# Kernel tuning notes

Measured on AMD Instinct MI355X. Metric: run time of the kernel, lower is better.

The kernel has to match this reference:

```python
import jax, jax.numpy as jnp
import numpy as np

B, L, ENC, D, H, HD, MLP, R = 4, 512, 512, 1024, 16, 64, 4096, 32
NUM_BUCKETS, MAX_DISTANCE = 32, 128
EPS = 1e-6
NEG = -1e10


def rmsnorm(x, scale):
    var = jnp.mean(jnp.square(x), axis=-1, keepdims=True)
    return x * jax.lax.rsqrt(var + EPS) * scale


def rel_pos_bias(table, qlen, klen):
    # T5 causal (bidirectional=False) relative position bucketing.
    ctx = jnp.arange(qlen)[:, None]
    mem = jnp.arange(klen)[None, :]
    rp = mem - ctx                      # [q, k]
    n = -jnp.minimum(rp, 0)             # distance into the past
    max_exact = NUM_BUCKETS // 2
    is_small = n < max_exact
    large = max_exact + (
        jnp.log(jnp.maximum(n, 1).astype(jnp.float32) / max_exact)
        / np.log(MAX_DISTANCE / max_exact) * (NUM_BUCKETS - max_exact)
    ).astype(jnp.int32)
    large = jnp.minimum(large, NUM_BUCKETS - 1)
    bucket = jnp.where(is_small, n, large)
    return table[bucket].transpose(2, 0, 1)[None]  # [1, h, q, k]


def lora_dense(x, W, a, b):
    # x:[B,L,d]  W:[d,e]  a:[B,d,r]  b:[B,r,e]  -> xW + (xa)b per example
    out = jnp.einsum('bld,de->ble', x, W)
    low = jnp.einsum('bld,bdr->blr', x, a)
    return out + jnp.einsum('blr,bre->ble', low, b)


def attention(xq, xkv, Wq, Wk, Wv, Wo, qa, qb, ka, kb, va, vb, oa, ob, bias):
    b, ql, _ = xq.shape
    kl = xkv.shape[1]
    q = lora_dense(xq, Wq, qa, qb).reshape(b, ql, H, HD) * (1.0 / np.sqrt(HD))
    k = lora_dense(xkv, Wk, ka, kb).reshape(b, kl, H, HD)
    v = lora_dense(xkv, Wv, va, vb).reshape(b, kl, H, HD)
    scores = jnp.einsum('bqhd,bkhd->bhqk', q, k)
    if bias is not None:
        scores = scores + bias
    probs = jax.nn.softmax(scores, axis=-1)
    ctx = jnp.einsum('bhqk,bkhd->bqhd', probs, v).reshape(b, ql, H * HD)
    return lora_dense(ctx, Wo, oa, ob)


def setup_inputs() -> dict:
    key = jax.random.key(0)
    ks = jax.random.split(key, 32)
    s = 0.02
    inp = {
        'inputs':  jax.random.normal(ks[0], (B, L, D), jnp.float32),
        'encoded': jax.random.normal(ks[1], (B, ENC, D), jnp.float32),
        'lora_qa': jax.random.normal(ks[2], (B, 2, D, R), jnp.float32) * s,
        'lora_qb': jax.random.normal(ks[3], (B, 2, R, D), jnp.float32) * s,
        'lora_ka': jax.random.normal(ks[4], (B, 2, D, R), jnp.float32) * s,
        'lora_kb': jax.random.normal(ks[5], (B, 2, R, D), jnp.float32) * s,
        'lora_va': jax.random.normal(ks[6], (B, 2, D, R), jnp.float32) * s,
        'lora_vb': jax.random.normal(ks[7], (B, 2, R, D), jnp.float32) * s,
        'lora_oa': jax.random.normal(ks[8], (B, 2, D, R), jnp.float32) * s,
        'lora_ob': jax.random.normal(ks[9], (B, 2, R, D), jnp.float32) * s,
        'rel_table': jax.random.normal(ks[10], (NUM_BUCKETS, H), jnp.float32) * s,
        'ln1': jnp.ones((D,), jnp.float32),
        'ln2': jnp.ones((D,), jnp.float32),
        'ln3': jnp.ones((D,), jnp.float32),
        'sWq': jax.random.normal(ks[11], (D, H * HD), jnp.float32) * s,
        'sWk': jax.random.normal(ks[12], (D, H * HD), jnp.float32) * s,
        'sWv': jax.random.normal(ks[13], (D, H * HD), jnp.float32) * s,
        'sWo': jax.random.normal(ks[14], (H * HD, D), jnp.float32) * s,
        'cWq': jax.random.normal(ks[15], (D, H * HD), jnp.float32) * s,
        'cWk': jax.random.normal(ks[16], (D, H * HD), jnp.float32) * s,
        'cWv': jax.random.normal(ks[17], (D, H * HD), jnp.float32) * s,
        'cWo': jax.random.normal(ks[18], (H * HD, D), jnp.float32) * s,
        'wi0': jax.random.normal(ks[19], (D, MLP), jnp.float32) * s,
        'wi1': jax.random.normal(ks[20], (D, MLP), jnp.float32) * s,
        'wo_mlp': jax.random.normal(ks[21], (MLP, D), jnp.float32) * s,
    }
    return inp


def reference(inputs, encoded, lora_qa, lora_qb, lora_ka, lora_kb, lora_va, lora_vb,
              lora_oa, lora_ob, rel_table, ln1, ln2, ln3,
              sWq, sWk, sWv, sWo, cWq, cWk, cWv, cWo, wi0, wi1, wo_mlp):
    l = inputs.shape[1]
    causal = jnp.tril(jnp.ones((l, l), dtype=bool))
    dec_bias = rel_pos_bias(rel_table, l, l) + jnp.where(causal, 0.0, NEG)[None, None]

    # --- self-attention block ---
    x = rmsnorm(inputs, ln1)
    x = attention(x, x, sWq, sWk, sWv, sWo,
                  lora_qa[:, 0], lora_qb[:, 0], lora_ka[:, 0], lora_kb[:, 0],
                  lora_va[:, 0], lora_vb[:, 0], lora_oa[:, 0], lora_ob[:, 0],
                  dec_bias)
    x = x + inputs

    # --- cross-attention block ---
    y = rmsnorm(x, ln2)
    y = attention(y, encoded, cWq, cWk, cWv, cWo,
                  lora_qa[:, 1], lora_qb[:, 1], lora_ka[:, 1], lora_kb[:, 1],
                  lora_va[:, 1], lora_vb[:, 1], lora_oa[:, 1], lora_ob[:, 1],
                  None)
    y = y + x

    # --- gated-gelu MLP block (T5 v1.1 style) ---
    lz = rmsnorm(y, ln3)
    h = jax.nn.gelu(lz @ wi0, approximate=False) * (lz @ wi1)
    z = h @ wo_mlp + y
    return z
```

## Files before the change

### kernel.cpp

```cpp
#include <hip/hip_runtime.h>
#include <math.h>


#define DEV __device__ __forceinline__

typedef __bf16 bf16x8 __attribute__((ext_vector_type(8)));
typedef float floatx4 __attribute__((ext_vector_type(4)));

typedef __attribute__((address_space(1))) void* gas_ptr;
typedef __attribute__((address_space(3))) void* las_ptr;

DEV unsigned short f2bf(float f) {
  union { float f; unsigned int u; } v; v.f = f;
  unsigned int r = v.u + 0x7fffu + ((v.u >> 16) & 1u);
  return (unsigned short)(r >> 16);
}
DEV float bf2f(unsigned short u) {
  union { unsigned int u; float f; } v; v.u = ((unsigned int)u) << 16;
  return v.f;
}

#define GLOAD_LDS16(g, l) __builtin_amdgcn_global_load_lds((gas_ptr)(g), (las_ptr)(l), 16, 0, 0)

template<int NW>
DEV void stage_tile_sw(const char* gbase, char* lds, int nrows, int ldbytes, int wave, int lane) {
  int nchunks = nrows >> 3;
  int colb = (((lane & 7) ^ ((lane >> 3) & 7)) << 4);
  for (int c = wave; c < nchunks; c += NW) {
    int row = (c << 3) + (lane >> 3);
    GLOAD_LDS16(gbase + (size_t)row * ldbytes + colb, lds + (c << 10));
  }
}

template<int NW>
DEV void stage_tile256_sw(const char* gbase, char* lds, int nrows, int ldbytes, int wave, int lane) {
  int nchunks = nrows >> 2;
  for (int c = wave; c < nchunks; c += NW) {
    int row = (c << 2) + (lane >> 4);
    int key = row & 7;
    int colb = ((lane & 15) ^ key) << 4;
    GLOAD_LDS16(gbase + (size_t)row * ldbytes + colb, lds + (c << 10));
  }
}

template<int WM, int WN>
DEV void gemm_core(const unsigned short* A, const unsigned short* Bt, float* C,
                   int K, int lda, int ldb, int ldc, int m0, int n0,
                   char* ldsA, char* ldsB) {
  constexpr int NW = WM * WN;
  const int tid  = threadIdx.x;
  const int lane = tid & 63;
  const int wave = tid >> 6;
  const int wm   = wave % WM;
  const int wn   = wave / WM;
  const int quad = lane >> 4;
  const int l15  = lane & 15;
  const int key  = l15 & 7;

  floatx4 acc[4][4];
#pragma unroll
  for (int i = 0; i < 4; ++i)
#pragma unroll
    for (int j = 0; j < 4; ++j) acc[i][j] = (floatx4){0.f, 0.f, 0.f, 0.f};

  const char* gA = (const char*)(A + (size_t)m0 * lda);
  const char* gB = (const char*)(Bt + (size_t)n0 * ldb);

  for (int k0 = 0; k0 < K; k0 += 64) {
    stage_tile_sw<NW>(gA + (size_t)k0 * 2, ldsA, WM * 64, lda * 2, wave, lane);
    stage_tile_sw<NW>(gB + (size_t)k0 * 2, ldsB, WN * 64, ldb * 2, wave, lane);
    __syncthreads();
#pragma unroll
    for (int kk = 0; kk < 64; kk += 32) {
      bf16x8 af[4], bv[4];
      int off = (((kk >> 3) + quad) ^ key) << 4;
      const char* baseA = ldsA + (size_t)(wm * 64 + l15) * 128 + off;
      const char* baseB = ldsB + (size_t)(wn * 64 + l15) * 128 + off;
#pragma unroll
      for (int mi = 0; mi < 4; ++mi) af[mi] = *(const bf16x8*)(baseA + mi * 2048);
#pragma unroll
      for (int ni = 0; ni < 4; ++ni) bv[ni] = *(const bf16x8*)(baseB + ni * 2048);
#pragma unroll
      for (int mi = 0; mi < 4; ++mi)
#pragma unroll
        for (int ni = 0; ni < 4; ++ni)
          acc[mi][ni] = __builtin_amdgcn_mfma_f32_16x16x32_bf16(af[mi], bv[ni], acc[mi][ni], 0, 0, 0);
    }
    __syncthreads();
  }

#pragma unroll
  for (int mi = 0; mi < 4; ++mi) {
#pragma unroll
    for (int r = 0; r < 4; ++r) {
      int row = m0 + wm * 64 + mi * 16 + quad * 4 + r;
#pragma unroll
// ... 51 lines not shown
      stage_tile_sw<4>((const char*)sl.A0 + (size_t)m0 * 2048 + it * 128, ldsA, 128, 2048, wave, lane);
      stage_tile_sw<4>((const char*)sl.B0 + (size_t)n0 * 2048 + it * 128, ldsB, 128, 2048, wave, lane);
    } else {
      int eb = (it - 16) * 128;
      stage_tile_sw<4>((const char*)sl.Aext + (size_t)m0 * 256 + eb, ldsA, 128, 256, wave, lane);
      stage_tile_sw<4>((const char*)(sl.Bext + (size_t)b * sl.bextb) + (size_t)n0 * 256 + eb,
                       ldsB, 128, 256, wave, lane);
    }
    __syncthreads();
#pragma unroll
    for (int kk = 0; kk < 64; kk += 32) {
      bf16x8 af[4], bv[4];
      int off = (((kk >> 3) + quad) ^ key) << 4;
      const char* baseA = ldsA + (size_t)(wm * 64 + l15) * 128 + off;
      const char* baseB = ldsB + (size_t)(wn * 64 + l15) * 128 + off;
#pragma unroll
      for (int mi = 0; mi < 4; ++mi) af[mi] = *(const bf16x8*)(baseA + mi * 2048);
#pragma unroll
      for (int ni = 0; ni < 4; ++ni) bv[ni] = *(const bf16x8*)(baseB + ni * 2048);
#pragma unroll
      for (int mi = 0; mi < 4; ++mi)
#pragma unroll
        for (int ni = 0; ni < 4; ++ni)
          acc[mi][ni] = __builtin_amdgcn_mfma_f32_16x16x32_bf16(af[mi], bv[ni], acc[mi][ni], 0, 0, 0);
    }
    __syncthreads();
  }

#pragma unroll
  for (int mi = 0; mi < 4; ++mi) {
#pragma unroll
    for (int r = 0; r < 4; ++r) {
      int row = m0 + wm * 64 + mi * 16 + quad * 4 + r;
#pragma unroll
      for (int ni = 0; ni < 4; ++ni) {
        int col = n0 + wn * 64 + ni * 16 + l15;
        sl.C[(size_t)row * sl.ldc + col] = acc[mi][ni][r];
      }
    }
  }
}

struct QKVSlice {
  const unsigned short* A0;
  const unsigned short* Aext;
  const unsigned short* B0;
  const unsigned short* Bext;
  unsigned short* sec0;
  unsigned short* sec1;
  unsigned short* sec2;
  size_t bextb;
  int vsec, nxa;
};
struct QKV2 { QKVSlice s[2]; };

__global__ __launch_bounds__(256) void k_gemmqkv(QKV2 g) {
  __shared__ char lds[34816];
  char* ldsA = lds;
  char* ldsB = lds + 16384;
  QKVSlice sl = g.s[blockIdx.z];
  if ((int)blockIdx.x >= sl.nxa) return;
  const int m0 = blockIdx.y * 128, n0 = blockIdx.x * 128;
  const int b = m0 >> 9;
  const int tid = threadIdx.x, lane = tid & 63, wave = tid >> 6;
  const int wm = wave & 1, wn = wave >> 1;
  const int quad = lane >> 4, l15 = lane & 15;
  const int key = l15 & 7;

  floatx4 acc[4][4];
#pragma unroll
  for (int i = 0; i < 4; ++i)
#pragma unroll
    for (int j = 0; j < 4; ++j) acc[i][j] = (floatx4){0.f, 0.f, 0.f, 0.f};

  for (int it = 0; it < 18; ++it) {
    if (it < 16) {
      stage_tile_sw<4>((const char*)sl.A0 + (size_t)m0 * 2048 + it * 128, ldsA, 128, 2048, wave, lane);
      stage_tile_sw<4>((const char*)sl.B0 + (size_t)n0 * 2048 + it * 128, ldsB, 128, 2048, wave, lane);
    } else {
      int eb = (it - 16) * 128;
      stage_tile_sw<4>((const char*)sl.Aext + (size_t)m0 * 256 + eb, ldsA, 128, 256, wave, lane);
      stage_tile_sw<4>((const char*)(sl.Bext + (size_t)b * sl.bextb) + (size_t)n0 * 256 + eb,
                       ldsB, 128, 256, wave, lane);
    }
    __syncthreads();
#pragma unroll
    for (int kk = 0; kk < 64; kk += 32) {
      bf16x8 af[4], bv[4];
      int off = (((kk >> 3) + quad) ^ key) << 4;
      const char* baseA = ldsA + (size_t)(wm * 64 + l15) * 128 + off;
      const char* baseB = ldsB + (size_t)(wn * 64 + l15) * 128 + off;
#pragma unroll
      for (int mi = 0; mi < 4; ++mi) af[mi] = *(const bf16x8*)(baseA + mi * 2048);
#pragma unroll
      for (int ni = 0; ni < 4; ++ni) bv[ni] = *(const bf16x8*)(baseB + ni * 2048);
#pragma unroll
      for (int mi = 0; mi < 4; ++mi)
#pragma unroll
        for (int ni = 0; ni < 4; ++ni)
          acc[mi][ni] = __builtin_amdgcn_mfma_f32_16x16x32_bf16(af[mi], bv[ni], acc[mi][ni], 0, 0, 0);
    }
    __syncthreads();
  }

  const int sec = n0 >> 10;
  const int nloc = n0 & 1023;
  if (sec != sl.vsec) {
    unsigned short* dst = (sec == 0) ? sl.sec0 : sl.sec1;
#pragma unroll
    for (int mi = 0; mi < 4; ++mi)
#pragma unroll
      for (int r = 0; r < 4; ++r) {
        int row = m0 + wm * 64 + mi * 16 + quad * 4 + r;
        unsigned short* drow = dst + (size_t)row * 1024 + nloc + wn * 64;
#pragma unroll
        for (int ni = 0; ni < 4; ++ni)
          drow[ni * 16 + l15] = f2bf(acc[mi][ni][r]);
      }
  } else {
    unsigned short* vdstb = (sl.vsec == 1) ? sl.sec1 : sl.sec2;
    char* vbuf = lds + (size_t)(wm * 2 + wn) * 8704;
#pragma unroll
    for (int ni = 0; ni < 4; ++ni)
#pragma unroll
      for (int mi = 0; mi < 4; ++mi) {
        unsigned long long pk =
            (unsigned long long)f2bf(acc[mi][ni][0])
          | ((unsigned long long)f2bf(acc[mi][ni][1]) << 16)
          | ((unsigned long long)f2bf(acc[mi][ni][2]) << 32)
          | ((unsigned long long)f2bf(acc[mi][ni][3]) << 48);
        *(unsigned long long*)(vbuf + (size_t)(ni * 16 + l15) * 136 + (mi * 16 + quad * 4) * 2) = pk;
      }
    __syncthreads();
    int dbase = nloc + wn * 64;
    int h = dbase >> 6;
    int kb = (m0 & 511) + wm * 64;
    unsigned short* vdst = vdstb + (size_t)(b * 16 + h) * 64 * 512;
    int lh = lane >> 3, ll = lane & 7;
#pragma unroll
    for (int i = 0; i < 8; ++i) {
      int d = i * 8 + lh;
      const char* p = vbuf + (size_t)d * 136 + ll * 16;
      unsigned long long lo = *(const unsigned long long*)p;
      unsigned long long hi = *(const unsigned long long*)(p + 8);
      uint4 v;
      v.x = (unsigned)lo; v.y = (unsigned)(lo >> 32);
      v.z = (unsigned)hi; v.w = (unsigned)(hi >> 32);
      *(uint4*)(vdst + (size_t)d * 512 + kb + ll * 8) = v;
    }
  }
}

template<bool CAUSAL, bool QSUM>
__global__ __launch_bounds__(256) void k_flash(const unsigned short* qmat, const float* qparts,
                                               const unsigned short* kmat, const unsigned short* vt,
                                               const float* rb, unsigned short* ctxb) {
  __shared__ char ldsQ[8192];
  __shared__ char ldsK[16384];
  __shared__ char ldsV[16384];
  __shared__ char ldsP[16384];
  __shared__ float lrb[512];

  const size_t PART = (size_t)2048 * 1024;
  const int z = blockIdx.y, b = z >> 4, h = z & 15;
  const int q0 = blockIdx.x * 64;
  const int tid = threadIdx.x, lane = tid & 63, wave = tid >> 6;
  const int quad = lane >> 4, l15 = lane & 15;
  const int key = l15 & 7;

  const unsigned short* K = kmat + (size_t)b * 512 * 1024 + h * 64;
  const unsigned short* V = vt + (size_t)z * 64 * 512;

  if (QSUM) {
#pragma unroll
    for (int rr = 0; rr < 4; ++rr) {
      int row = rr * 16 + (tid >> 4);
      int c4 = tid & 15;
      const float* src = qparts + (size_t)(q0 + row) * 1024 + h * 64 + c4 * 4;
      float4 s0 = *(const float4*)src;
      float4 s1 = *(const float4*)(src + PART);
      float4 s2 = *(const float4*)(src + 2 * PART);
      float4 s3 = *(const float4*)(src + 3 * PART);
      ushort4 o;
      o.x = f2bf(s0.x + s1.x + s2.x + s3.x);
      o.y = f2bf(s0.y + s1.y + s2.y + s3.y);
      o.z = f2bf(s0.z + s1.z + s2.z + s3.z);
      o.w = f2bf(s0.w + s1.w + s2.w + s3.w);
      int qoff = (((c4 >> 1) ^ (row & 7)) << 4) | ((c4 & 1) << 3);
      *(ushort4*)(ldsQ + (size_t)row * 128 + qoff) = o;
    }
  } else {
    const unsigned short* Q = qmat + (size_t)b * 512 * 1024 + h * 64;
    stage_tile_sw<4>((const char*)(Q + (size_t)q0 * 1024), ldsQ, 64, 2048, wave, lane);
  }
  if (CAUSAL)
    for (int i = tid; i < 512; i += 256) lrb[i] = rb[h * 512 + i];

  float m_run[4], l_run[4];
  floatx4 oacc[4];
#pragma unroll
  for (int r = 0; r < 4; ++r) { m_run[r] = -1e30f; l_run[r] = 0.f; }
#pragma unroll
  for (int ni = 0; ni < 4; ++ni) oacc[ni] = (floatx4){0.f, 0.f, 0.f, 0.f};

  const int ktend = CAUSAL ? (blockIdx.x / 2 + 1) : 4;
  for (int kt = 0; kt < ktend; ++kt) {
    __syncthreads();
    stage_tile_sw<4>((const char*)(K + (size_t)kt * 128 * 1024), ldsK, 128, 2048, wave, lane);
    stage_tile256_sw<4>((const char*)(V + kt * 128), ldsV, 64, 1024, wave, lane);
    __syncthreads();

    floatx4 sacc[8];
#pragma unroll
    for (int ct = 0; ct < 8; ++ct) sacc[ct] = (floatx4){0.f, 0.f, 0.f, 0.f};
    const size_t qrow = (size_t)(wave * 16 + l15) * 128;
#pragma unroll
    for (int kd = 0; kd < 2; ++kd) {
      int offq = ((quad + kd * 4) ^ key) << 4;
      bf16x8 af = *(const bf16x8*)(ldsQ + qrow + offq);
// ... 120 lines not shown
    __syncthreads();
#pragma unroll
    for (int kk = 0; kk < 64; kk += 32) {
      bf16x8 af[4], bv[4];
      int off = (((kk >> 3) + quad) ^ key) << 4;
      const char* baseA = ldsA + (size_t)(wm * 64 + l15) * 128 + off;
      const char* baseB = ldsB + (size_t)(half * 128 + wn * 64 + l15) * 128 + off;
#pragma unroll
      for (int mi = 0; mi < 4; ++mi) af[mi] = *(const bf16x8*)(baseA + mi * 2048);
#pragma unroll
      for (int ni = 0; ni < 4; ++ni) bv[ni] = *(const bf16x8*)(baseB + ni * 2048);
#pragma unroll
      for (int mi = 0; mi < 4; ++mi)
#pragma unroll
        for (int ni = 0; ni < 4; ++ni)
          acc[mi][ni] = __builtin_amdgcn_mfma_f32_16x16x32_bf16(af[mi], bv[ni], acc[mi][ni], 0, 0, 0);
    }
    __syncthreads();
  }

  if (half == 1) {
#pragma unroll
    for (int mi = 0; mi < 4; ++mi)
#pragma unroll
      for (int r = 0; r < 4; ++r) {
        int row = wm * 64 + mi * 16 + quad * 4 + r;
#pragma unroll
        for (int ni = 0; ni < 4; ++ni) {
          int col = wn * 64 + ni * 16 + l15;
          *(unsigned short*)(ldsB + (size_t)row * 256 + col * 2) = f2bf(acc[mi][ni][r]);
        }
      }
  }
  __syncthreads();
  if (half == 0) {
#pragma unroll
    for (int mi = 0; mi < 4; ++mi)
#pragma unroll
      for (int r = 0; r < 4; ++r) {
        int row = wm * 64 + mi * 16 + quad * 4 + r;
#pragma unroll
        for (int ni = 0; ni < 4; ++ni) {
          int col = wn * 64 + ni * 16 + l15;
          float h1 = bf2f(*(const unsigned short*)(ldsB + (size_t)row * 256 + col * 2));
          float g = acc[mi][ni][r];
          float v = 0.5f * g * (1.0f + erff(g * 0.70710678f)) * h1;
          hbf[(size_t)(m0 + row) * 4096 + n0 + col] = f2bf(v);
        }
      }
  }
}

struct PrepArgs {
  const float* src[11];
  unsigned short* dst[11];
  int K[11], N[11], mode[11];
  int tstart[12];
  const float* encoded;
  unsigned short* encbf;
  const float* table;
  float* rb;
  unsigned short* bmdst[5];
  const float* bmsrc[5][3];
  int bmnrg[5];
  int bmstart[6];
  int nwt, nf2bf, nbm;
  const float* xin; const float* ln1;
  const float* qa; const float* ka; const float* va;
  unsigned short* xnp; unsigned short* lows;
  const float* lca0; const float* lca1;
  unsigned short* lowc;
};
__global__ __launch_bounds__(256, 2) void k_prep(PrepArgs a) {
  __shared__ char shm[33792];
  int bid = blockIdx.x;
  int t = threadIdx.x;
  if (bid < 256) {
    unsigned short (*lrows)[1024] = (unsigned short(*)[1024])shm;
    float* pacc = (float*)(shm + 16384);
    float* red  = (float*)(shm + 28672);
    int row0 = bid * 8;
    int b = row0 >> 9;
    float4 s4 = ((const float4*)a.ln1)[t];
    for (int j = 0; j < 8; ++j) {
      int row = row0 + j;
      float4 v = ((const float4*)(a.xin + (size_t)row * 1024))[t];
      float ss = v.x * v.x + v.y * v.y + v.z * v.z + v.w * v.w;
      for (int o = 32; o; o >>= 1) ss += __shfl_down(ss, o);
      if ((t & 63) == 0) red[t >> 6] = ss;
      __syncthreads();
      float tot = red[0] + red[1] + red[2] + red[3];
      float rs = rsqrtf(tot * (1.0f / 1024.0f) + 1e-6f);
      ushort4 o;
      o.x = f2bf(v.x * rs * s4.x); o.y = f2bf(v.y * rs * s4.y);
      o.z = f2bf(v.z * rs * s4.z); o.w = f2bf(v.w * rs * s4.w);
      ((ushort4*)(a.xnp + (size_t)row * 1024))[t] = o;
      *(ushort4*)(&lrows[j][t * 4]) = o;
      __syncthreads();
    }
    int r = t & 31, g = t >> 5;
    float acc[3][8];
#pragma unroll
    for (int p = 0; p < 3; ++p)
#pragma unroll
      for (int j = 0; j < 8; ++j) acc[p][j] = 0.f;
    const float* aq = a.qa + (size_t)b * 65536;
    const float* ak = a.ka + (size_t)b * 65536;
    const float* av = a.va + (size_t)b * 65536;
    for (int i = 0; i < 128; ++i) {
      int k = g * 128 + i;
// ... 101 lines not shown
    for (int cg = 0; cg < 16; cg += 8) {
      float vv[8][4];
#pragma unroll
      for (int cc = 0; cc < 8; ++cc)
#pragma unroll
        for (int e = 0; e < 4; ++e) {
          int c = coff + (cg + cc) * 4 + e;
          vv[cc][e] = ((c >> 5) == sec) ? src[(size_t)(c & 31) * 1024 + ncol] : 0.f;
        }
#pragma unroll
      for (int cc = 0; cc < 8; ++cc) {
        ushort4 o;
        o.x = f2bf(vv[cc][0]); o.y = f2bf(vv[cc][1]);
        o.z = f2bf(vv[cc][2]); o.w = f2bf(vv[cc][3]);
        *(ushort4*)(drow + (cg + cc) * 4) = o;
      }
    }
    return;
  }
  bid -= a.nbm;
  if (bid < 32) {
    int i = bid * 256 + t;
    if (i < 16 * 512) {
      int h = i >> 9, d = i & 511;
      int bucket;
      if (d < 16) bucket = d;
      else {
        int lb = 16 + (int)(logf((float)d / 16.0f) / logf(8.0f) * 16.0f);
        bucket = lb < 31 ? lb : 31;
      }
      a.rb[i] = a.table[bucket * 16 + h];
    }
    return;
  }
  bid -= 32;
  if (bid < a.nf2bf) {
    const float4* src = (const float4*)a.encoded;
    ushort4* dst = (ushort4*)a.encbf;
    int base = bid * 2048 + t;
    float4 v[8];
#pragma unroll
    for (int i = 0; i < 8; ++i) v[i] = src[base + i * 256];
#pragma unroll
    for (int i = 0; i < 8; ++i) {
      ushort4 o;
      o.x = f2bf(v[i].x); o.y = f2bf(v[i].y); o.z = f2bf(v[i].z); o.w = f2bf(v[i].w);
      dst[base + i * 256] = o;
    }
    return;
  }
  bid -= a.nf2bf;
  {
    int z = 0;
    while (z < 10 && bid >= a.tstart[z + 1]) ++z;
    int tile = bid - a.tstart[z];
    int N = a.N[z], K = a.K[z], mode = a.mode[z];
    int ntn = N >> 7;
    int tn = tile % ntn, tk = tile / ntn;
    const float* src = a.src[z] + (size_t)(tk * 128) * N + tn * 128;
#pragma unroll
    for (int i = 0; i < 4; ++i) {
      int c = i * 256 + t;
      int k4 = c >> 5;
      int c4 = c & 31;
      const float* p = src + (size_t)(k4 * 4) * N + c4 * 4;
      float4 v0 = *(const float4*)(p);
      float4 v1 = *(const float4*)(p + N);
      float4 v2 = *(const float4*)(p + 2 * (size_t)N);
      float4 v3 = *(const float4*)(p + 3 * (size_t)N);
      char* base = shm + (size_t)(c4 * 4) * 264 + k4 * 8;
      ushort4 o;
      o.x = f2bf(v0.x); o.y = f2bf(v1.x); o.z = f2bf(v2.x); o.w = f2bf(v3.x);
      *(ushort4*)(base) = o;
      o.x = f2bf(v0.y); o.y = f2bf(v1.y); o.z = f2bf(v2.y); o.w = f2bf(v3.y);
      *(ushort4*)(base + 264) = o;
      o.x = f2bf(v0.z); o.y = f2bf(v1.z); o.z = f2bf(v2.z); o.w = f2bf(v3.z);
      *(ushort4*)(base + 528) = o;
      o.x = f2bf(v0.w); o.y = f2bf(v1.w); o.z = f2bf(v2.w); o.w = f2bf(v3.w);
      *(ushort4*)(base + 792) = o;
    }
    __syncthreads();
    {
      int g2 = t >> 4, j = t & 15;
#pragma unroll
      for (int rr = 0; rr < 8; ++rr) {
        int nl = rr * 16 + g2;
        int n = tn * 128 + nl;
        int orow = (mode == 0) ? n : ((n >> 7) * 256 + ((mode == 2) ? 128 : 0) + (n & 127));
        const char* p = shm + (size_t)nl * 264 + j * 16;
        unsigned long long lo = *(const unsigned long long*)p;
        unsigned long long hi = *(const unsigned long long*)(p + 8);
        uint4 v;
        v.x = (unsigned)lo; v.y = (unsigned)(lo >> 32);
        v.z = (unsigned)hi; v.w = (unsigned)(hi >> 32);
        *(uint4*)(a.dst[z] + (size_t)orow * K + tk * 128 + j * 8) = v;
      }
    }
  }
}

template<bool LOW>
__global__ __launch_bounds__(256) void k_addbrms(const float* parts, const float* resid,
                                                 const float* sc, float* resout,
                                                 unsigned short* xn,
                                                 const float* aP, unsigned short* lowext) {
  __shared__ unsigned short lrows[8][1024];
  __shared__ float pacc[8 * 8 * 32];
  __shared__ float red[4];
  const size_t PART = (size_t)2048 * 1024;
  int t = threadIdx.x;
  int row0 = blockIdx.x * 8;
  int b = row0 >> 9;
  float4 s4 = ((const float4*)sc)[t];
  for (int j = 0; j < 8; ++j) {
    int row = row0 + j;
    const float* p0 = parts + (size_t)row * 1024;
    float4 v = ((const float4*)p0)[t];
    float4 v1 = ((const float4*)(p0 + PART))[t];
    float4 v2 = ((const float4*)(p0 + 2 * PART))[t];
    float4 v3 = ((const float4*)(p0 + 3 * PART))[t];
    float4 rv = ((const float4*)(resid + (size_t)row * 1024))[t];
    float4 s;
    s.x = v.x + v1.x + v2.x + v3.x + rv.x;
    s.y = v.y + v1.y + v2.y + v3.y + rv.y;
    s.z = v.z + v1.z + v2.z + v3.z + rv.z;
    s.w = v.w + v1.w + v2.w + v3.w + rv.w;
    ((float4*)(resout + (size_t)row * 1024))[t] = s;
    float ss = s.x * s.x + s.y * s.y + s.z * s.z + s.w * s.w;
    for (int o = 32; o; o >>= 1) ss += __shfl_down(ss, o);
    if ((t & 63) == 0) red[t >> 6] = ss;
    __syncthreads();
    float tot = red[0] + red[1] + red[2] + red[3];
    float rs = rsqrtf(tot * (1.0f / 1024.0f) + 1e-6f);
    ushort4 o;
    o.x = f2bf(s.x * rs * s4.x); o.y = f2bf(s.y * rs * s4.y);
    o.z = f2bf(s.z * rs * s4.z); o.w = f2bf(s.w * rs * s4.w);
    ((ushort4*)(xn + (size_t)row * 1024))[t] = o;
    if (LOW) *(ushort4*)(&lrows[j][t * 4]) = o;
    __syncthreads();
  }
  if (LOW) {
    int r = t & 31, g = t >> 5;
    float acc[8];
#pragma unroll
    for (int j = 0; j < 8; ++j) acc[j] = 0.f;
    const float* ap = aP + (size_t)b * 65536;
    for (int i = 0; i < 128; ++i) {
      int k = g * 128 + i;
      float a0 = ap[(size_t)k * 32 + r];
#pragma unroll
// ... 69 lines not shown
  const float* f_ln2 = (const float*)d_in[12];
  const float* f_ln3 = (const float*)d_in[13];
  const float* f_W[8] = { (const float*)d_in[14], (const float*)d_in[15],
                          (const float*)d_in[16], (const float*)d_in[17],
                          (const float*)d_in[18], (const float*)d_in[19],
                          (const float*)d_in[20], (const float*)d_in[21] };
  const float* f_wi0 = (const float*)d_in[22];
  const float* f_wi1 = (const float*)d_in[23];
  const float* f_wo  = (const float*)d_in[24];

  const size_t SEL1 = 32768;
  const size_t PART = (size_t)2048 * 1024;

  char* w = (char*)d_ws;
  size_t off = 0;
  auto alloc = [&](size_t bytes) -> char* {
    off = (off + 255) & ~(size_t)255;
    char* p = w + off;
    off += bytes;
    return p;
  };
  unsigned short* wt  = (unsigned short*)alloc((size_t)8192 * 1024 * 2);
  unsigned short* wc  = (unsigned short*)alloc((size_t)8192 * 1024 * 2);
  unsigned short* wot = (unsigned short*)alloc((size_t)1024 * 4096 * 2);
  unsigned short* encbf = (unsigned short*)alloc(2048 * 1024 * 2);
  float* rb = (float*)alloc(16 * 512 * 4);
  unsigned short* xn  = (unsigned short*)alloc(2048 * 1024 * 2);
  unsigned short* qbf = (unsigned short*)alloc(2048 * 1024 * 2);
  unsigned short* kbf = (unsigned short*)alloc(2048 * 1024 * 2);
  unsigned short* vtb = (unsigned short*)alloc((size_t)64 * 64 * 512 * 2);
  unsigned short* kbf2 = (unsigned short*)alloc(2048 * 1024 * 2);
  unsigned short* vtb2 = (unsigned short*)alloc((size_t)64 * 64 * 512 * 2);
  unsigned short* lowext_s = (unsigned short*)alloc(2048 * 128 * 2);
  unsigned short* lowext_c = (unsigned short*)alloc(2048 * 128 * 2);
  unsigned short* lowext_q = (unsigned short*)alloc(2048 * 128 * 2);
  unsigned short* lowext_o = (unsigned short*)alloc(2048 * 128 * 2);
  unsigned short* bmext_s  = (unsigned short*)alloc((size_t)4 * 3072 * 128 * 2);
  unsigned short* bmext_c  = (unsigned short*)alloc((size_t)4 * 2048 * 128 * 2);
  unsigned short* bmext_q  = (unsigned short*)alloc((size_t)4 * 1024 * 128 * 2);
  unsigned short* bmext_o  = (unsigned short*)alloc((size_t)4 * 1024 * 128 * 2);
  unsigned short* bmext_o2 = (unsigned short*)alloc((size_t)4 * 1024 * 128 * 2);
  unsigned short* ctxb = (unsigned short*)alloc(2048 * 1024 * 2);
  float* xres = (float*)alloc(2048 * 1024 * 4);
  float* yres = (float*)alloc(2048 * 1024 * 4);
  char*  big  = alloc((size_t)84 << 20);
  float* op_s = (float*)big;
  float* qp_c = (float*)(big + ((size_t)32 << 20));
  float* op_c = (float*)big;
  unsigned short* hbf = (unsigned short*)big;
  float* fp   = (float*)(big + ((size_t)16 << 20));
  (void)ws_size; (void)in_sizes; (void)n_in; (void)out_size;

  PrepArgs pa;
  int ts = 0;
  for (int i = 0; i < 8; ++i) {
    pa.src[i] = f_W[i]; pa.dst[i] = wt + (size_t)i * 1024 * 1024;
    pa.K[i] = 1024; pa.N[i] = 1024; pa.mode[i] = 0;
    pa.tstart[i] = ts; ts += 64;
  }
  pa.src[8] = f_wi0; pa.dst[8] = wc; pa.K[8] = 1024; pa.N[8] = 4096; pa.mode[8] = 1;
  pa.tstart[8] = ts; ts += 256;
  pa.src[9] = f_wi1; pa.dst[9] = wc; pa.K[9] = 1024; pa.N[9] = 4096; pa.mode[9] = 2;
  pa.tstart[9] = ts; ts += 256;
  pa.src[10] = f_wo; pa.dst[10] = wot; pa.K[10] = 4096; pa.N[10] = 1024; pa.mode[10] = 0;
  pa.tstart[10] = ts; ts += 256;
  pa.tstart[11] = ts;
  pa.nwt = ts;
  pa.encoded = f_encoded; pa.encbf = encbf;
  pa.table = f_table; pa.rb = rb;
  pa.nf2bf = 256;
  pa.bmdst[0] = bmext_s;  pa.bmnrg[0] = 24;
  pa.bmsrc[0][0] = f_qb; pa.bmsrc[0][1] = f_kb; pa.bmsrc[0][2] = f_vb;
  pa.bmdst[1] = bmext_c;  pa.bmnrg[1] = 16;
  pa.bmsrc[1][0] = f_kb + SEL1; pa.bmsrc[1][1] = f_vb + SEL1; pa.bmsrc[1][2] = nullptr;
  pa.bmdst[2] = bmext_q;  pa.bmnrg[2] = 8;
  pa.bmsrc[2][0] = f_qb + SEL1; pa.bmsrc[2][1] = nullptr; pa.bmsrc[2][2] = nullptr;
  pa.bmdst[3] = bmext_o;  pa.bmnrg[3] = 8;
  pa.bmsrc[3][0] = f_ob; pa.bmsrc[3][1] = nullptr; pa.bmsrc[3][2] = nullptr;
  pa.bmdst[4] = bmext_o2; pa.bmnrg[4] = 8;
  pa.bmsrc[4][0] = f_ob + SEL1; pa.bmsrc[4][1] = nullptr; pa.bmsrc[4][2] = nullptr;
  int bs = 0;
  for (int m = 0; m < 5; ++m) { pa.bmstart[m] = bs; bs += pa.bmnrg[m] * 4; }
  pa.bmstart[5] = bs;
  pa.nbm = bs;
  pa.xin = f_inputs; pa.ln1 = f_ln1;
  pa.qa = f_qa; pa.ka = f_ka; pa.va = f_va;
  pa.xnp = xn; pa.lows = lowext_s;
  pa.lca0 = f_ka + SEL1; pa.lca1 = f_va + SEL1;
  pa.lowc = lowext_c;
  int totblk = 512 + pa.nbm + 32 + pa.nf2bf + pa.nwt;
  k_prep<<<dim3(totblk), dim3(256), 0, stream>>>(pa);

  {
    QKV2 g;
    g.s[0] = { xn, lowext_s, wt, bmext_s,
               qbf, kbf, vtb, (size_t)3072 * 128, 2, 24 };
    g.s[1] = { encbf, lowext_c, wt + (size_t)5120 * 1024, bmext_c,
               kbf2, vtb2, nullptr, (size_t)2048 * 128, 1, 16 };
    k_gemmqkv<<<dim3(24, 16, 2), dim3(256), 0, stream>>>(g);
  }

  k_flash<true, false><<<dim3(8, 64), dim3(256), 0, stream>>>(qbf, nullptr, kbf, vtb, rb, ctxb);

  k_lowbf<<<dim3(256), dim3(256), 0, stream>>>(ctxb, f_oa, lowext_o);
  {
    GX g;
    for (int s = 0; s < 4; ++s)
      g.s[s] = { ctxb, lowext_o, wt + (size_t)3072 * 1024, bmext_o, op_s + (size_t)s * PART,
                 (size_t)1024 * 128, 1024, 8, s * 18 / 4, (s + 1) * 18 / 4 };
    k_gemmx<<<dim3(8, 16, 4), dim3(256), 0, stream>>>(g);
  }
  k_addbrms<true><<<dim3(256), dim3(256), 0, stream>>>(op_s, f_inputs, f_ln2, xres, xn,
                                                       f_qa + SEL1, lowext_q);

  {
    GX g;
    for (int s = 0; s < 4; ++s)
      g.s[s] = { xn, lowext_q, wt + (size_t)4096 * 1024, bmext_q, qp_c + (size_t)s * PART,
                 (size_t)1024 * 128, 1024, 8, s * 18 / 4, (s + 1) * 18 / 4 };
    k_gemmx<<<dim3(8, 16, 4), dim3(256), 0, stream>>>(g);
  }
  k_flash<false, true><<<dim3(8, 64), dim3(256), 0, stream>>>(nullptr, qp_c, kbf2, vtb2, rb, ctxb);

  k_lowbf<<<dim3(256), dim3(256), 0, stream>>>(ctxb, f_oa + SEL1, lowext_o);
  {
    GX g;
    for (int s = 0; s < 4; ++s)
      g.s[s] = { ctxb, lowext_o, wt + (size_t)7168 * 1024, bmext_o2, op_c + (size_t)s * PART,
                 (size_t)1024 * 128, 1024, 8, s * 18 / 4, (s + 1) * 18 / 4 };
    k_gemmx<<<dim3(8, 16, 4), dim3(256), 0, stream>>>(g);
  }
  k_addbrms<false><<<dim3(256), dim3(256), 0, stream>>>(op_c, xres, f_ln3, yres, xn,
                                                        nullptr, nullptr);

  k_mlp<<<dim3(32, 16), dim3(512), 0, stream>>>(xn, wc, hbf);
  k_gemm1s<<<dim3(8, 16, 4), dim3(256), 0, stream>>>(hbf, wot, fp, PART, 1024, 4096, 4096, 1024);
  k_sum4<<<dim3(2048), dim3(256), 0, stream>>>(fp, PART, yres, (float*)d_out);
}
```

Measured before the change: 507.7 us.

## Move late-use weight transposes from prep kernel into QKV GEMM launch

Splits the fp32-to-bf16 weight transpose work. Only the weights needed by the first QKV GEMM (self q/k/v and cross k/v) stay in the prep kernel. The transposes for the output projections, cross-q and the MLP weights become extra z-slices of the QKV GEMM grid, so they run alongside the GEMM tiles. This shortens the critical-path prep kernel and fills spare CUs during the GEMM, at the cost of contending with the GEMM for memory bandwidth.

```diff
diff --git a/kernel.cpp b/kernel.cpp
--- a/kernel.cpp
+++ b/kernel.cpp
@@ -40,6 +40,50 @@
     int key = row & 7;
     int colb = ((lane & 15) ^ key) << 4;
     GLOAD_LDS16(gbase + (size_t)row * ldbytes + colb, lds + (c << 10));
+  }
+}
+
+DEV void transpose_tile128(const float* src0, unsigned short* dst,
+                           int N, int K, int mode, int tn, int tk,
+                           char* shm, int t) {
+  const float* src = src0 + (size_t)(tk * 128) * N + tn * 128;
+#pragma unroll
+  for (int i = 0; i < 4; ++i) {
+    int c = i * 256 + t;
+    int k4 = c >> 5;
+    int c4 = c & 31;
+    const float* p = src + (size_t)(k4 * 4) * N + c4 * 4;
+    float4 v0 = *(const float4*)(p);
+    float4 v1 = *(const float4*)(p + N);
+    float4 v2 = *(const float4*)(p + 2 * (size_t)N);
+    float4 v3 = *(const float4*)(p + 3 * (size_t)N);
+    char* base = shm + (size_t)(c4 * 4) * 264 + k4 * 8;
+    ushort4 o;
+    o.x = f2bf(v0.x); o.y = f2bf(v1.x); o.z = f2bf(v2.x); o.w = f2bf(v3.x);
+    *(ushort4*)(base) = o;
+    o.x = f2bf(v0.y); o.y = f2bf(v1.y); o.z = f2bf(v2.y); o.w = f2bf(v3.y);
+    *(ushort4*)(base + 264) = o;
+    o.x = f2bf(v0.z); o.y = f2bf(v1.z); o.z = f2bf(v2.z); o.w = f2bf(v3.z);
+    *(ushort4*)(base + 528) = o;
+    o.x = f2bf(v0.w); o.y = f2bf(v1.w); o.z = f2bf(v2.w); o.w = f2bf(v3.w);
+    *(ushort4*)(base + 792) = o;
+  }
+  __syncthreads();
+  {
+    int g2 = t >> 4, j = t & 15;
+#pragma unroll
+    for (int rr = 0; rr < 8; ++rr) {
+      int nl = rr * 16 + g2;
+      int n = tn * 128 + nl;
+      int orow = (mode == 0) ? n : ((n >> 7) * 256 + ((mode == 2) ? 128 : 0) + (n & 127));
+      const char* p = shm + (size_t)nl * 264 + j * 16;
+      unsigned long long lo = *(const unsigned long long*)p;
+      unsigned long long hi = *(const unsigned long long*)(p + 8);
+      uint4 v;
+      v.x = (unsigned)lo; v.y = (unsigned)(lo >> 32);
+      v.z = (unsigned)hi; v.w = (unsigned)(hi >> 32);
+      *(uint4*)(dst + (size_t)orow * K + tk * 128 + j * 8) = v;
+    }
   }
 }
 
@@ -199,17 +243,37 @@
   size_t bextb;
   int vsec, nxa;
 };
-struct QKV2 { QKVSlice s[2]; };
-
-__global__ __launch_bounds__(256) void k_gemmqkv(QKV2 g) {
+struct QKVT {
+  QKVSlice s[2];
+  const float* tsrc[6];
+  unsigned short* tdst[6];
+  int tK[6], tN[6], tmode[6];
+  int tstart[7];
+  int ntt;
+};
+
+__global__ __launch_bounds__(256) void k_gemmqkv(QKVT g) {
   __shared__ char lds[34816];
   char* ldsA = lds;
   char* ldsB = lds + 16384;
+  const int tid = threadIdx.x;
+  if (blockIdx.z >= 2) {
+    int bid = (blockIdx.z - 2) * 384 + blockIdx.y * 24 + blockIdx.x;
+    if (bid >= g.ntt) return;
+    int z = 0;
+    while (z < 5 && bid >= g.tstart[z + 1]) ++z;
+    int tile = bid - g.tstart[z];
+    int N = g.tN[z], K = g.tK[z];
+    int ntn = N >> 7;
+    transpose_tile128(g.tsrc[z], g.tdst[z], N, K, g.tmode[z],
+                      tile % ntn, tile / ntn, lds, tid);
+    return;
+  }
   QKVSlice sl = g.s[blockIdx.z];
   if ((int)blockIdx.x >= sl.nxa) return;
   const int m0 = blockIdx.y * 128, n0 = blockIdx.x * 128;
   const int b = m0 >> 9;
-  const int tid = threadIdx.x, lane = tid & 63, wave = tid >> 6;
+  const int lane = tid & 63, wave = tid >> 6;
   const int wm = wave & 1, wn = wave >> 1;
   const int quad = lane >> 4, l15 = lane & 15;
   const int key = l15 & 7;
@@ -538,10 +602,9 @@
 }
 
 struct PrepArgs {
-  const float* src[11];
-  unsigned short* dst[11];
-  int K[11], N[11], mode[11];
-  int tstart[12];
+  const float* src[5];
+  unsigned short* dst[5];
+  int tstart[6];
   const float* encoded;
   unsigned short* encbf;
   const float* table;
@@ -749,50 +812,10 @@
   bid -= a.nf2bf;
   {
     int z = 0;
-    while (z < 10 && bid >= a.tstart[z + 1]) ++z;
+    while (z < 4 && bid >= a.tstart[z + 1]) ++z;
     int tile = bid - a.tstart[z];
-    int N = a.N[z], K = a.K[z], mode = a.mode[z];
-    int ntn = N >> 7;
-    int tn = tile % ntn, tk = tile / ntn;
-    const float* src = a.src[z] + (size_t)(tk * 128) * N + tn * 128;
-#pragma unroll
-    for (int i = 0; i < 4; ++i) {
-      int c = i * 256 + t;
-      int k4 = c >> 5;
-      int c4 = c & 31;
-      const float* p = src + (size_t)(k4 * 4) * N + c4 * 4;
-      float4 v0 = *(const float4*)(p);
-      float4 v1 = *(const float4*)(p + N);
-      float4 v2 = *(const float4*)(p + 2 * (size_t)N);
-      float4 v3 = *(const float4*)(p + 3 * (size_t)N);
-      char* base = shm + (size_t)(c4 * 4) * 264 + k4 * 8;
-      ushort4 o;
-      o.x = f2bf(v0.x); o.y = f2bf(v1.x); o.z = f2bf(v2.x); o.w = f2bf(v3.x);
-      *(ushort4*)(base) = o;
-      o.x = f2bf(v0.y); o.y = f2bf(v1.y); o.z = f2bf(v2.y); o.w = f2bf(v3.y);
-      *(ushort4*)(base + 264) = o;
-      o.x = f2bf(v0.z); o.y = f2bf(v1.z); o.z = f2bf(v2.z); o.w = f2bf(v3.z);
-      *(ushort4*)(base + 528) = o;
-      o.x = f2bf(v0.w); o.y = f2bf(v1.w); o.z = f2bf(v2.w); o.w = f2bf(v3.w);
-      *(ushort4*)(base + 792) = o;
-    }
-    __syncthreads();
-    {
-      int g2 = t >> 4, j = t & 15;
-#pragma unroll
-      for (int rr = 0; rr < 8; ++rr) {
-        int nl = rr * 16 + g2;
-        int n = tn * 128 + nl;
-        int orow = (mode == 0) ? n : ((n >> 7) * 256 + ((mode == 2) ? 128 : 0) + (n & 127));
-        const char* p = shm + (size_t)nl * 264 + j * 16;
-        unsigned long long lo = *(const unsigned long long*)p;
-        unsigned long long hi = *(const unsigned long long*)(p + 8);
-        uint4 v;
-        v.x = (unsigned)lo; v.y = (unsigned)(lo >> 32);
-        v.z = (unsigned)hi; v.w = (unsigned)(hi >> 32);
-        *(uint4*)(a.dst[z] + (size_t)orow * K + tk * 128 + j * 8) = v;
-      }
-    }
+    transpose_tile128(a.src[z], a.dst[z], 1024, 1024, 0,
+                      tile & 7, tile >> 3, shm, t);
   }
 }
 
@@ -968,20 +991,18 @@
   (void)ws_size; (void)in_sizes; (void)n_in; (void)out_size;
 
   PrepArgs pa;
-  int ts = 0;
-  for (int i = 0; i < 8; ++i) {
-    pa.src[i] = f_W[i]; pa.dst[i] = wt + (size_t)i * 1024 * 1024;
-    pa.K[i] = 1024; pa.N[i] = 1024; pa.mode[i] = 0;
-    pa.tstart[i] = ts; ts += 64;
-  }
-  pa.src[8] = f_wi0; pa.dst[8] = wc; pa.K[8] = 1024; pa.N[8] = 4096; pa.mode[8] = 1;
-  pa.tstart[8] = ts; ts += 256;
-  pa.src[9] = f_wi1; pa.dst[9] = wc; pa.K[9] = 1024; pa.N[9] = 4096; pa.mode[9] = 2;
-  pa.tstart[9] = ts; ts += 256;
-  pa.src[10] = f_wo; pa.dst[10] = wot; pa.K[10] = 4096; pa.N[10] = 1024; pa.mode[10] = 0;
-  pa.tstart[10] = ts; ts += 256;
-  pa.tstart[11] = ts;
-  pa.nwt = ts;
+  {
+    const float* wsrc5[5] = { f_W[0], f_W[1], f_W[2], f_W[5], f_W[6] };
+    const int slot5[5] = { 0, 1, 2, 5, 6 };
+    int ts = 0;
+    for (int i = 0; i < 5; ++i) {
+      pa.src[i] = wsrc5[i];
+      pa.dst[i] = wt + (size_t)slot5[i] * 1024 * 1024;
+      pa.tstart[i] = ts; ts += 64;
+    }
+    pa.tstart[5] = ts;
+    pa.nwt = ts;
+  }
   pa.encoded = f_encoded; pa.encbf = encbf;
   pa.table = f_table; pa.rb = rb;
   pa.nf2bf = 256;
@@ -1008,12 +1029,27 @@
   k_prep<<<dim3(totblk), dim3(256), 0, stream>>>(pa);
 
   {
-    QKV2 g;
+    QKVT g;
     g.s[0] = { xn, lowext_s, wt, bmext_s,
                qbf, kbf, vtb, (size_t)3072 * 128, 2, 24 };
     g.s[1] = { encbf, lowext_c, wt + (size_t)5120 * 1024, bmext_c,
                kbf2, vtb2, nullptr, (size_t)2048 * 128, 1, 16 };
-    k_gemmqkv<<<dim3(24, 16, 2), dim3(256), 0, stream>>>(g);
+    const float* tsrc[6] = { f_W[3], f_W[4], f_W[7], f_wi0, f_wi1, f_wo };
+    unsigned short* tdst[6] = { wt + (size_t)3072 * 1024, wt + (size_t)4096 * 1024,
+                                wt + (size_t)7168 * 1024, wc, wc, wot };
+    int tK[6] = { 1024, 1024, 1024, 1024, 1024, 4096 };
+    int tN[6] = { 1024, 1024, 1024, 4096, 4096, 1024 };
+    int tmode[6] = { 0, 0, 0, 1, 2, 0 };
+    int ts2 = 0;
+    for (int i = 0; i < 6; ++i) {
+      g.tsrc[i] = tsrc[i]; g.tdst[i] = tdst[i];
+      g.tK[i] = tK[i]; g.tN[i] = tN[i]; g.tmode[i] = tmode[i];
+      g.tstart[i] = ts2;
+      ts2 += (tK[i] >> 7) * (tN[i] >> 7);
+    }
+    g.tstart[6] = ts2;
+    g.ntt = ts2;
+    k_gemmqkv<<<dim3(24, 16, 5), dim3(256), 0, stream>>>(g);
   }
 
   k_flash<true, false><<<dim3(8, 64), dim3(256), 0, stream>>>(qbf, nullptr, kbf, vtb, rb, ctxb);
```

Result: no change. 506.9 us (-0.1%).

## Defer later-needed weight transposes into the causal flash-attention launch

Applied to the files above, without the earlier changes.

Moves the fp32-to-bf16 transposes of weights not needed until later (self-attn Wo, cross Wq, cross Wo, MLP wo) out of the prep kernel and into extra blocks (blockIdx.z==1) of the first flash-attention launch. This shortens the prep kernel on the critical path and lets the transpose work fill idle CUs while the causal attention runs. In exchange, the flash kernel now uses a single merged shared buffer and carries a larger argument struct, and the extra blocks compete with attention blocks for bandwidth and CU slots.

```diff
diff --git a/kernel.cpp b/kernel.cpp
--- a/kernel.cpp
+++ b/kernel.cpp
@@ -42,6 +42,58 @@
     GLOAD_LDS16(gbase + (size_t)row * ldbytes + colb, lds + (c << 10));
   }
 }
+
+DEV void transpose_tile128(const float* src0, unsigned short* dst,
+                           int N, int K, int mode, int tn, int tk,
+                           char* shm, int t) {
+  const float* src = src0 + (size_t)(tk * 128) * N + tn * 128;
+#pragma unroll
+  for (int i = 0; i < 4; ++i) {
+    int c = i * 256 + t;
+    int k4 = c >> 5;
+    int c4 = c & 31;
+    const float* p = src + (size_t)(k4 * 4) * N + c4 * 4;
+    float4 v0 = *(const float4*)(p);
+    float4 v1 = *(const float4*)(p + N);
+    float4 v2 = *(const float4*)(p + 2 * (size_t)N);
+    float4 v3 = *(const float4*)(p + 3 * (size_t)N);
+    char* base = shm + (size_t)(c4 * 4) * 264 + k4 * 8;
+    ushort4 o;
+    o.x = f2bf(v0.x); o.y = f2bf(v1.x); o.z = f2bf(v2.x); o.w = f2bf(v3.x);
+    *(ushort4*)(base) = o;
+    o.x = f2bf(v0.y); o.y = f2bf(v1.y); o.z = f2bf(v2.y); o.w = f2bf(v3.y);
+    *(ushort4*)(base + 264) = o;
+    o.x = f2bf(v0.z); o.y = f2bf(v1.z); o.z = f2bf(v2.z); o.w = f2bf(v3.z);
+    *(ushort4*)(base + 528) = o;
+    o.x = f2bf(v0.w); o.y = f2bf(v1.w); o.z = f2bf(v2.w); o.w = f2bf(v3.w);
+    *(ushort4*)(base + 792) = o;
+  }
+  __syncthreads();
+  {
+    int g2 = t >> 4, j = t & 15;
+#pragma unroll
+    for (int rr = 0; rr < 8; ++rr) {
+      int nl = rr * 16 + g2;
+      int n = tn * 128 + nl;
+      int orow = (mode == 0) ? n : ((n >> 7) * 256 + ((mode == 2) ? 128 : 0) + (n & 127));
+      const char* p = shm + (size_t)nl * 264 + j * 16;
+      unsigned long long lo = *(const unsigned long long*)p;
+      unsigned long long hi = *(const unsigned long long*)(p + 8);
+      uint4 v;
+      v.x = (unsigned)lo; v.y = (unsigned)(lo >> 32);
+      v.z = (unsigned)hi; v.w = (unsigned)(hi >> 32);
+      *(uint4*)(dst + (size_t)orow * K + tk * 128 + j * 8) = v;
+    }
+  }
+}
+
+struct TJob {
+  const float* tsrc[4];
+  unsigned short* tdst[4];
+  int tK[4], tN[4];
+  int tstart[5];
+  int ntt;
+};
 
 template<int WM, int WN>
 DEV void gemm_core(const unsigned short* A, const unsigned short* Bt, float* C,
@@ -301,17 +353,31 @@
 template<bool CAUSAL, bool QSUM>
 __global__ __launch_bounds__(256) void k_flash(const unsigned short* qmat, const float* qparts,
                                                const unsigned short* kmat, const unsigned short* vt,
-                                               const float* rb, unsigned short* ctxb) {
-  __shared__ char ldsQ[8192];
-  __shared__ char ldsK[16384];
-  __shared__ char ldsV[16384];
-  __shared__ char ldsP[16384];
-  __shared__ float lrb[512];
+                                               const float* rb, unsigned short* ctxb, TJob tj) {
+  __shared__ char shm[59392];
+  char* ldsQ = shm;
+  char* ldsK = shm + 8192;
+  char* ldsV = shm + 24576;
+  char* ldsP = shm + 40960;
+  float* lrb = (float*)(shm + 57344);
+
+  const int tid = threadIdx.x;
+  if (blockIdx.z == 1) {
+    int bid = blockIdx.y * gridDim.x + blockIdx.x;
+    if (bid >= tj.ntt) return;
+    int z = 0;
+    while (z < 3 && bid >= tj.tstart[z + 1]) ++z;
+    int tile = bid - tj.tstart[z];
+    int ntn = tj.tN[z] >> 7;
+    transpose_tile128(tj.tsrc[z], tj.tdst[z], tj.tN[z], tj.tK[z], 0,
+                      tile % ntn, tile / ntn, shm, tid);
+    return;
+  }
 
   const size_t PART = (size_t)2048 * 1024;
   const int z = blockIdx.y, b = z >> 4, h = z & 15;
   const int q0 = blockIdx.x * 64;
-  const int tid = threadIdx.x, lane = tid & 63, wave = tid >> 6;
+  const int lane = tid & 63, wave = tid >> 6;
   const int quad = lane >> 4, l15 = lane & 15;
   const int key = l15 & 7;
 
@@ -538,10 +604,10 @@
 }
 
 struct PrepArgs {
-  const float* src[11];
-  unsigned short* dst[11];
-  int K[11], N[11], mode[11];
-  int tstart[12];
+  const float* src[7];
+  unsigned short* dst[7];
+  int tK[7], tN[7], tmode[7];
+  int tstart[8];
   const float* encoded;
   unsigned short* encbf;
   const float* table;
@@ -749,50 +815,11 @@
   bid -= a.nf2bf;
   {
     int z = 0;
-    while (z < 10 && bid >= a.tstart[z + 1]) ++z;
+    while (z < 6 && bid >= a.tstart[z + 1]) ++z;
     int tile = bid - a.tstart[z];
-    int N = a.N[z], K = a.K[z], mode = a.mode[z];
-    int ntn = N >> 7;
-    int tn = tile % ntn, tk = tile / ntn;
-    const float* src = a.src[z] + (size_t)(tk * 128) * N + tn * 128;
-#pragma unroll
-    for (int i = 0; i < 4; ++i) {
-      int c = i * 256 + t;
-      int k4 = c >> 5;
-      int c4 = c & 31;
-      const float* p = src + (size_t)(k4 * 4) * N + c4 * 4;
-      float4 v0 = *(const float4*)(p);
-      float4 v1 = *(const float4*)(p + N);
-      float4 v2 = *(const float4*)(p + 2 * (size_t)N);
-      float4 v3 = *(const float4*)(p + 3 * (size_t)N);
-      char* base = shm + (size_t)(c4 * 4) * 264 + k4 * 8;
-      ushort4 o;
-      o.x = f2bf(v0.x); o.y = f2bf(v1.x); o.z = f2bf(v2.x); o.w = f2bf(v3.x);
-      *(ushort4*)(base) = o;
-      o.x = f2bf(v0.y); o.y = f2bf(v1.y); o.z = f2bf(v2.y); o.w = f2bf(v3.y);
-      *(ushort4*)(base + 264) = o;
-      o.x = f2bf(v0.z); o.y = f2bf(v1.z); o.z = f2bf(v2.z); o.w = f2bf(v3.z);
-      *(ushort4*)(base + 528) = o;
-      o.x = f2bf(v0.w); o.y = f2bf(v1.w); o.z = f2bf(v2.w); o.w = f2bf(v3.w);
-      *(ushort4*)(base + 792) = o;
-    }
-    __syncthreads();
-    {
-      int g2 = t >> 4, j = t & 15;
-#pragma unroll
-      for (int rr = 0; rr < 8; ++rr) {
-        int nl = rr * 16 + g2;
-        int n = tn * 128 + nl;
-        int orow = (mode == 0) ? n : ((n >> 7) * 256 + ((mode == 2) ? 128 : 0) + (n & 127));
-        const char* p = shm + (size_t)nl * 264 + j * 16;
-        unsigned long long lo = *(const unsigned long long*)p;
-        unsigned long long hi = *(const unsigned long long*)(p + 8);
-        uint4 v;
-        v.x = (unsigned)lo; v.y = (unsigned)(lo >> 32);
-        v.z = (unsigned)hi; v.w = (unsigned)(hi >> 32);
-        *(uint4*)(a.dst[z] + (size_t)orow * K + tk * 128 + j * 8) = v;
-      }
-    }
+    int ntn = a.tN[z] >> 7;
+    transpose_tile128(a.src[z], a.dst[z], a.tN[z], a.tK[z], a.tmode[z],
+                      tile % ntn, tile / ntn, shm, t);
   }
 }
 
@@ -968,20 +995,24 @@
   (void)ws_size; (void)in_sizes; (void)n_in; (void)out_size;
 
   PrepArgs pa;
-  int ts = 0;
-  for (int i = 0; i < 8; ++i) {
-    pa.src[i] = f_W[i]; pa.dst[i] = wt + (size_t)i * 1024 * 1024;
-    pa.K[i] = 1024; pa.N[i] = 1024; pa.mode[i] = 0;
-    pa.tstart[i] = ts; ts += 64;
-  }
-  pa.src[8] = f_wi0; pa.dst[8] = wc; pa.K[8] = 1024; pa.N[8] = 4096; pa.mode[8] = 1;
-  pa.tstart[8] = ts; ts += 256;
-  pa.src[9] = f_wi1; pa.dst[9] = wc; pa.K[9] = 1024; pa.N[9] = 4096; pa.mode[9] = 2;
-  pa.tstart[9] = ts; ts += 256;
-  pa.src[10] = f_wo; pa.dst[10] = wot; pa.K[10] = 4096; pa.N[10] = 1024; pa.mode[10] = 0;
-  pa.tstart[10] = ts; ts += 256;
-  pa.tstart[11] = ts;
-  pa.nwt = ts;
+  {
+    const float* wsrc7[7] = { f_W[0], f_W[1], f_W[2], f_W[5], f_W[6], f_wi0, f_wi1 };
+    unsigned short* wdst7[7] = { wt, wt + (size_t)1024 * 1024, wt + (size_t)2048 * 1024,
+                                 wt + (size_t)5120 * 1024, wt + (size_t)6144 * 1024,
+                                 wc, wc };
+    int tK7[7] = { 1024, 1024, 1024, 1024, 1024, 1024, 1024 };
+    int tN7[7] = { 1024, 1024, 1024, 1024, 1024, 4096, 4096 };
+    int tm7[7] = { 0, 0, 0, 0, 0, 1, 2 };
+    int ts = 0;
+    for (int i = 0; i < 7; ++i) {
+      pa.src[i] = wsrc7[i]; pa.dst[i] = wdst7[i];
+      pa.tK[i] = tK7[i]; pa.tN[i] = tN7[i]; pa.tmode[i] = tm7[i];
+      pa.tstart[i] = ts;
+      ts += (tK7[i] >> 7) * (tN7[i] >> 7);
+    }
+    pa.tstart[7] = ts;
+    pa.nwt = ts;
+  }
   pa.encoded = f_encoded; pa.encbf = encbf;
   pa.table = f_table; pa.rb = rb;
   pa.nf2bf = 256;
@@ -1016,7 +1047,25 @@
     k_gemmqkv<<<dim3(24, 16, 2), dim3(256), 0, stream>>>(g);
   }
 
-  k_flash<true, false><<<dim3(8, 64), dim3(256), 0, stream>>>(qbf, nullptr, kbf, vtb, rb, ctxb);
+  {
+    TJob tj;
+    const float* fsrc[4] = { f_W[3], f_W[4], f_W[7], f_wo };
+    unsigned short* fdst[4] = { wt + (size_t)3072 * 1024, wt + (size_t)4096 * 1024,
+                                wt + (size_t)7168 * 1024, wot };
+    int fK[4] = { 1024, 1024, 1024, 4096 };
+    int fN[4] = { 1024, 1024, 1024, 1024 };
+    int ts = 0;
+    for (int i = 0; i < 4; ++i) {
+      tj.tsrc[i] = fsrc[i]; tj.tdst[i] = fdst[i];
+      tj.tK[i] = fK[i]; tj.tN[i] = fN[i];
+      tj.tstart[i] = ts;
+      ts += (fK[i] >> 7) * (fN[i] >> 7);
+    }
+    tj.tstart[4] = ts;
+    tj.ntt = ts;
+    k_flash<true, false><<<dim3(8, 64, 2), dim3(256), 0, stream>>>(
+        qbf, nullptr, kbf, vtb, rb, ctxb, tj);
+  }
 
   k_lowbf<<<dim3(256), dim3(256), 0, stream>>>(ctxb, f_oa, lowext_o);
   {
@@ -1036,7 +1085,16 @@
                  (size_t)1024 * 128, 1024, 8, s * 18 / 4, (s + 1) * 18 / 4 };
     k_gemmx<<<dim3(8, 16, 4), dim3(256), 0, stream>>>(g);
   }
-  k_flash<false, true><<<dim3(8, 64), dim3(256), 0, stream>>>(nullptr, qp_c, kbf2, vtb2, rb, ctxb);
+  {
+    TJob tj0;
+    for (int i = 0; i < 4; ++i) {
+      tj0.tsrc[i] = nullptr; tj0.tdst[i] = nullptr;
+      tj0.tK[i] = 0; tj0.tN[i] = 128; tj0.tstart[i] = 0;
+    }
+    tj0.tstart[4] = 0; tj0.ntt = 0;
+    k_flash<false, true><<<dim3(8, 64, 1), dim3(256), 0, stream>>>(
+        nullptr, qp_c, kbf2, vtb2, rb, ctxb, tj0);
+  }
 
   k_lowbf<<<dim3(256), dim3(256), 0, stream>>>(ctxb, f_oa + SEL1, lowext_o);
   {
```

After: 509.6 us (median of 2 runs). About the same (+0.4%).
